# Optimization experiments

Measured on AMD Instinct MI355X. Metric: run time of the kernel, lower is better.

The kernel has to match this reference:

```python
import jax, jax.numpy as jnp
import numpy as np

DIM = 256
NUM_HEADS = 8
HEAD_DIM = DIM // NUM_HEADS
SCALE = HEAD_DIM ** (-0.5)


def setup_inputs() -> dict:
    key = jax.random.key(0)
    k1, k2, k3, k4 = jax.random.split(key, 4)
    x = jax.random.normal(k1, (4, 1, DIM, 12, 12, 12), dtype=jnp.float32)
    w_qkv = jax.random.normal(k2, (3 * DIM, DIM), dtype=jnp.float32) * 0.02
    w_proj = jax.random.normal(k3, (DIM, DIM), dtype=jnp.float32) * 0.02
    b_proj = jax.random.normal(k4, (DIM,), dtype=jnp.float32) * 0.02
    return {"x": x, "w_qkv": w_qkv, "w_proj": w_proj, "b_proj": b_proj}


def reference(x, w_qkv, w_proj, b_proj):
    # x: [P=4, B, C, H, W, D]; 1x1x1 Conv3d == channel matmul
    P, B, C, H, W, D = x.shape
    N = H * W * D
    xf = x.reshape(P, B, C, N)                       # [P,B,C,N]
    qkv = jnp.einsum('pbcn,oc->pbon', xf, w_qkv)     # [P,B,3C,N]
    q, k, v = jnp.split(qkv, 3, axis=2)              # each [P,B,C,N]
    # fold batch*heads
    def heads(t):
        return t.reshape(P, B * NUM_HEADS, HEAD_DIM, N)
    q, k, v = heads(q) * SCALE, heads(k), heads(v)
    attn = jnp.einsum('phcm,phcn->phmn', q, k)       # [P,BH,N,N]
    attn = jax.nn.softmax(attn, axis=-1)
    out = jnp.einsum('phmn,phcn->phcm', attn, v)     # [P,BH,hd,N]
    out = out.reshape(P, B, C, N)
    out = jnp.einsum('pbcn,oc->pbon', out, w_proj) + b_proj[None, None, :, None]
    return out.reshape(P, B, C, H, W, D)
```

## Files before the change

### kernel.cpp

```cpp
#include <hip/hip_runtime.h>

#define NP 4
#define NH 8
#define HD 32
#define CD 256
#define NN 1728
#define NT_TILES 27
#define SCALE_Q2 (0.17677669529663687f * 1.4426950408889634f)

typedef __bf16 bf16x8 __attribute__((ext_vector_type(8)));
typedef __bf16 bf16x4_t __attribute__((ext_vector_type(4)));
typedef short short4_t __attribute__((ext_vector_type(4)));
typedef float f32x4 __attribute__((ext_vector_type(4)));
typedef unsigned short ushort4_t __attribute__((ext_vector_type(4)));
typedef unsigned short ushort8_t __attribute__((ext_vector_type(8)));

__device__ __forceinline__ float bf2f(unsigned short u) {
  unsigned int v = ((unsigned int)u) << 16;
  return __builtin_bit_cast(float, v);
}
__device__ __forceinline__ unsigned short f2bf(float f) {
  unsigned int v = __builtin_bit_cast(unsigned int, f);
  unsigned int r = (v + 0x7FFFu + ((v >> 16) & 1u)) >> 16;
  return (unsigned short)r;
}

__global__ void k_prep(const float* __restrict__ x, unsigned short* __restrict__ xt,
                       const float* __restrict__ wqkv, const float* __restrict__ wproj,
                       unsigned short* __restrict__ wq_b, unsigned short* __restrict__ wp_b) {
  __shared__ __attribute__((aligned(16))) unsigned short tile[64 * 40];
  int bid = blockIdx.x;
  int t = threadIdx.x;
  if (bid >= 864) {
    int idx = ((bid - 864) * 256 + t) * 4;
    const float* src;
    unsigned short* dst;
    if (idx < 196608) { src = wqkv + idx; dst = wq_b + idx; }
    else { src = wproj + (idx - 196608); dst = wp_b + (idx - 196608); }
    float4 v = *(const float4*)src;
    ushort4_t o;
    o[0] = f2bf(v.x); o[1] = f2bf(v.y); o[2] = f2bf(v.z); o[3] = f2bf(v.w);
    *(ushort4_t*)dst = o;
    return;
  }
  int nb = (bid % 27) * 64, cb = ((bid / 27) & 7) * 32, p = bid / 216;
  {
    int c = t >> 3, ch = t & 7;
    const float* src = x + ((size_t)p * CD + cb + c) * NN + nb + ch * 8;
    float4 v0 = *(const float4*)src;
    float4 v1 = *(const float4*)(src + 4);
    int base = ch * 8;
    tile[(base + 0) * 40 + c] = f2bf(v0.x);
    tile[(base + 1) * 40 + c] = f2bf(v0.y);
    tile[(base + 2) * 40 + c] = f2bf(v0.z);
    tile[(base + 3) * 40 + c] = f2bf(v0.w);
    tile[(base + 4) * 40 + c] = f2bf(v1.x);
    tile[(base + 5) * 40 + c] = f2bf(v1.y);
    tile[(base + 6) * 40 + c] = f2bf(v1.z);
    tile[(base + 7) * 40 + c] = f2bf(v1.w);
  }
  __syncthreads();
  {
    int n = t >> 2, ch = t & 3;
    *(ushort8_t*)(xt + ((size_t)p * NN + nb + n) * CD + cb + ch * 8) =
        *(const ushort8_t*)&tile[n * 40 + ch * 8];
  }
}

__global__ void k_qkv(const unsigned short* __restrict__ xt,
                      const unsigned short* __restrict__ wqkv,
                      unsigned short* __restrict__ Qt, unsigned short* __restrict__ Kt,
                      unsigned short* __restrict__ Vv) {
  int p = blockIdx.z, ot = blockIdx.y, nt = blockIdx.x;
  int tid = threadIdx.x, w = tid >> 6, lane = tid & 63, l15 = lane & 15, g = lane >> 4;
  int nbase = nt * 64 + w * 16;
  f32x4 acc[4] = {};
  const unsigned short* arow = xt + ((size_t)p * NN + nbase + l15) * CD + g * 8;
  const unsigned short* wrow = wqkv + ((size_t)(ot * 64 + l15)) * CD + g * 8;
  for (int ks = 0; ks < 8; ks++) {
    bf16x8 a = *(const bf16x8*)(arow + ks * 32);
#pragma unroll
    for (int ob = 0; ob < 4; ob++) {
      bf16x8 b = *(const bf16x8*)(wrow + ob * 16 * CD + ks * 32);
      acc[ob] = __builtin_amdgcn_mfma_f32_16x16x32_bf16(a, b, acc[ob], 0, 0, 0);
    }
  }
#pragma unroll
  for (int ob = 0; ob < 4; ob++) {
    int o = ot * 64 + ob * 16 + l15;
    int wq = o >> 8, rem = o & 255, h = rem >> 5, cc = rem & 31;
    int ph = p * NH + h;
    int nrow = nbase + g * 4;
    if (wq == 0) {
      for (int r = 0; r < 4; r++)
        Qt[((size_t)ph * NN + nrow + r) * HD + cc] = f2bf(acc[ob][r] * SCALE_Q2);
    } else if (wq == 1) {
      for (int r = 0; r < 4; r++)
        Kt[((size_t)ph * NN + nrow + r) * HD + cc] = f2bf(acc[ob][r]);
    } else {
      ushort4_t vs;
      for (int r = 0; r < 4; r++) vs[r] = f2bf(acc[ob][r]);
      *(ushort4_t*)(Vv + ((size_t)ph * HD + cc) * NN + nrow) = vs;
    }
  }
}

__global__ __launch_bounds__(256) void k_attn(const unsigned short* __restrict__ Qt,
                                              const unsigned short* __restrict__ Kt,
                                              const unsigned short* __restrict__ Vv,
                                              unsigned short* __restrict__ op0,
                                              unsigned short* __restrict__ op1,
                                              float* __restrict__ Lp) {
  __shared__ __attribute__((aligned(16))) unsigned char lds[2 * (5120 + 4096)];
  int tid = threadIdx.x, w = tid >> 6, lane = tid & 63, l15 = lane & 15, g = lane >> 4;
  int mt = blockIdx.x, ph = blockIdx.y, z = blockIdx.z;
  int t0 = z * 14, tEnd = z ? NT_TILES : 14;
  const unsigned short* qptr = Qt + ((size_t)ph * NN + mt * 64 + w * 16 + l15) * HD + g * 8;
  bf16x8 qfrag = *(const bf16x8*)qptr;
  const unsigned short* ktb = Kt + (size_t)ph * NN * HD;
  const unsigned short* vb = Vv + (size_t)ph * HD * NN;
  f32x4 lsum = {0.f, 0.f, 0.f, 0.f};
  f32x4 oacc[2] = {};
  int snl = tid >> 2, sch = tid & 3;
  int svc = tid >> 3, svch = tid & 7;
  const int kst_off = snl * 80 + sch * 16;
  const int vst_off = (svc * 128 + svch * 16) ^ ((svc & 7) << 4);
  f32x4 zacc = {0.f, 0.f, 0.f, 0.f};
  {
    ushort8_t kr = *(const ushort8_t*)(ktb + ((size_t)(t0 * 64 + snl)) * HD + sch * 8);
    ushort8_t vr = *(const ushort8_t*)(vb + (size_t)svc * NN + t0 * 64 + svch * 8);
    *(ushort8_t*)(lds + kst_off) = kr;
    *(ushort8_t*)(lds + 5120 + vst_off) = vr;
  }
  __syncthreads();
  for (int nt = t0; nt < tEnd; nt++) {
    unsigned char* kbuf = lds + (nt & 1) * 9216;
    unsigned char* vbuf = kbuf + 5120;
    unsigned char* kbufN = lds + ((nt + 1) & 1) * 9216;
    unsigned char* vbufN = kbufN + 5120;
    ushort8_t kr, vr;
    bool pre = (nt + 1 < tEnd);
    if (pre) {
      kr = *(const ushort8_t*)(ktb + ((size_t)((nt + 1) * 64 + snl)) * HD + sch * 8);
      vr = *(const ushort8_t*)(vb + (size_t)svc * NN + (nt + 1) * 64 + svch * 8);
    }
    f32x4 s[4];
#pragma unroll
    for (int nf = 0; nf < 4; nf++) {
      bf16x8 kb = *(const bf16x8*)(kbuf + (nf * 16 + l15) * 80 + g * 16);
      s[nf] = __builtin_amdgcn_mfma_f32_16x16x32_bf16(kb, qfrag, zacc, 0, 0, 0);
    }
    short4_t pa[4];
#pragma unroll
    for (int nf = 0; nf < 4; nf++) {
      f32x4 e;
#pragma unroll
      for (int r = 0; r < 4; r++) e[r] = __builtin_amdgcn_exp2f(s[nf][r]);
      lsum += e;
      bf16x4_t t;
#pragma unroll
      for (int r = 0; r < 4; r++) t[r] = (__bf16)e[r];
      pa[nf] = __builtin_bit_cast(short4_t, t);
    }
#pragma unroll
    for (int nf = 0; nf < 4; nf++) {
#pragma unroll
      for (int cb = 0; cb < 2; cb++) {
        int c = cb * 16 + l15;
        ushort4_t vq = *(const ushort4_t*)(vbuf + ((c * 128 + nf * 32 + g * 8) ^ ((c & 7) << 4)));
        short4_t va = __builtin_bit_cast(short4_t, vq);
        oacc[cb] = __builtin_amdgcn_mfma_f32_16x16x16bf16_1k(va, pa[nf], oacc[cb], 0, 0, 0);
      }
    }
    if (pre) {
      *(ushort8_t*)(kbufN + kst_off) = kr;
      *(ushort8_t*)(vbufN + vst_off) = vr;
    }
    __syncthreads();
  }
  float total = lsum[0] + lsum[1] + lsum[2] + lsum[3];
  total += __shfl_xor(total, 16);
  total += __shfl_xor(total, 32);
  int m = mt * 64 + w * 16 + l15;
  unsigned short* op = z ? op1 : op0;
  if (g == 0) Lp[(size_t)z * 32 * NN + (size_t)ph * NN + m] = total;
#pragma unroll
  for (int cb = 0; cb < 2; cb++) {
    ushort4_t vs;
#pragma unroll
    for (int rr = 0; rr < 4; rr++) vs[rr] = f2bf(oacc[cb][rr]);
    *(ushort4_t*)(op + ((size_t)ph * NN + m) * 32 + cb * 16 + g * 4) = vs;
  }
}

__global__ void k_proj(const unsigned short* __restrict__ op0,
                       const unsigned short* __restrict__ op1,
                       const float* __restrict__ Lp,
                       const unsigned short* __restrict__ wproj,
                       const float* __restrict__ bproj,
                       float* __restrict__ out) {
  int p = blockIdx.z, ot = blockIdx.y, nt = blockIdx.x;
  int tid = threadIdx.x, w = tid >> 6, lane = tid & 63, l15 = lane & 15, g = lane >> 4;
  int nbase = nt * 64 + w * 16;
  int n = nbase + l15;
  f32x4 acc[4] = {};
  const unsigned short* wrow = wproj + ((size_t)(ot * 64 + l15)) * CD + g * 8;
  for (int ks = 0; ks < 8; ks++) {
    size_t r = (size_t)(p * NH + ks) * NN + n;
    float inv = 1.0f / (Lp[r] + Lp[(size_t)32 * NN + r]);
    ushort8_t a0 = *(const ushort8_t*)(op0 + r * 32 + g * 8);
    ushort8_t a1 = *(const ushort8_t*)(op1 + r * 32 + g * 8);
    bf16x8 a;
#pragma unroll
    for (int j = 0; j < 8; j++) a[j] = (__bf16)((bf2f(a0[j]) + bf2f(a1[j])) * inv);
#pragma unroll
    for (int ob = 0; ob < 4; ob++) {
      bf16x8 b = *(const bf16x8*)(wrow + ob * 16 * CD + ks * 32);
      acc[ob] = __builtin_amdgcn_mfma_f32_16x16x32_bf16(a, b, acc[ob], 0, 0, 0);
    }
  }
#pragma unroll
  for (int ob = 0; ob < 4; ob++) {
    int o = ot * 64 + ob * 16 + l15;
    float bias = bproj[o];
    int nrow = nbase + g * 4;
    float4 vs;
    vs.x = acc[ob][0] + bias;
    vs.y = acc[ob][1] + bias;
    vs.z = acc[ob][2] + bias;
    vs.w = acc[ob][3] + bias;
    *(float4*)(out + (size_t)p * CD * NN + (size_t)o * NN + nrow) = vs;
  }
}

extern "C" void kernel_launch(void* const* d_in, const int* in_sizes, int n_in,
                              void* d_out, int out_size, void* d_ws, size_t ws_size,
                              hipStream_t stream) {
  const float* x = (const float*)d_in[0];
  const float* wqkv = (const float*)d_in[1];
  const float* wproj = (const float*)d_in[2];
  const float* bproj = (const float*)d_in[3];
  float* out = (float*)d_out;
  unsigned short* ws = (unsigned short*)d_ws;
  const size_t SZ = (size_t)NP * NN * CD;
  unsigned short* xt = ws;
  unsigned short* Qt = ws + SZ;
  unsigned short* Kt = ws + 2 * SZ;
  unsigned short* Vv = ws + 3 * SZ;
  unsigned short* op1 = ws + 4 * SZ;
  unsigned short* wq_b = ws + 5 * SZ;
  unsigned short* wp_b = ws + 5 * SZ + 196608;
  float* Lp = (float*)(ws + 5 * SZ + 262144);
  unsigned short* op0 = xt;
  hipLaunchKernelGGL(k_prep, dim3(1120), dim3(256), 0, stream, x, xt, wqkv, wproj, wq_b, wp_b);
  hipLaunchKernelGGL(k_qkv, dim3(27, 12, NP), dim3(256), 0, stream, xt, wq_b, Qt, Kt, Vv);
  hipLaunchKernelGGL(k_attn, dim3(27, 32, 2), dim3(256), 0, stream, Qt, Kt, Vv, op0, op1, Lp);
  hipLaunchKernelGGL(k_proj, dim3(27, 4, NP), dim3(256), 0, stream, op0, op1, Lp, wp_b, bproj, out);
}
```

Baseline: 80.20 us.

## Store V in MFMA fragment order and read K/V straight from global

The QKV projection now writes V in a tiled layout that matches the MFMA operand fragment order. The attention kernel drops its LDS double buffer and its per-tile __syncthreads, and loads K and V fragments directly from global memory, relying on cache since all four waves read the same tiles. This removes the LDS staging and barriers, but adds latency-exposed global loads inside the loop with no explicit prefetch.

```diff
diff --git a/kernel.cpp b/kernel.cpp
--- a/kernel.cpp
+++ b/kernel.cpp
@@ -100,7 +100,7 @@
     } else {
       ushort4_t vs;
       for (int r = 0; r < 4; r++) vs[r] = f2bf(acc[ob][r]);
-      *(ushort4_t*)(Vv + ((size_t)ph * HD + cc) * NN + nrow) = vs;
+      *(ushort4_t*)(Vv + (size_t)ph * 55296 + nt * 2048 + w * 512 + cc * 16 + g * 4) = vs;
     }
   }
 }
@@ -111,43 +111,21 @@
                                               unsigned short* __restrict__ op0,
                                               unsigned short* __restrict__ op1,
                                               float* __restrict__ Lp) {
-  __shared__ __attribute__((aligned(16))) unsigned char lds[2 * (5120 + 4096)];
   int tid = threadIdx.x, w = tid >> 6, lane = tid & 63, l15 = lane & 15, g = lane >> 4;
   int mt = blockIdx.x, ph = blockIdx.y, z = blockIdx.z;
   int t0 = z * 14, tEnd = z ? NT_TILES : 14;
   const unsigned short* qptr = Qt + ((size_t)ph * NN + mt * 64 + w * 16 + l15) * HD + g * 8;
   bf16x8 qfrag = *(const bf16x8*)qptr;
   const unsigned short* ktb = Kt + (size_t)ph * NN * HD;
-  const unsigned short* vb = Vv + (size_t)ph * HD * NN;
+  const unsigned short* vb = Vv + (size_t)ph * 55296;
   f32x4 lsum = {0.f, 0.f, 0.f, 0.f};
   f32x4 oacc[2] = {};
-  int snl = tid >> 2, sch = tid & 3;
-  int svc = tid >> 3, svch = tid & 7;
-  const int kst_off = snl * 80 + sch * 16;
-  const int vst_off = (svc * 128 + svch * 16) ^ ((svc & 7) << 4);
   f32x4 zacc = {0.f, 0.f, 0.f, 0.f};
-  {
-    ushort8_t kr = *(const ushort8_t*)(ktb + ((size_t)(t0 * 64 + snl)) * HD + sch * 8);
-    ushort8_t vr = *(const ushort8_t*)(vb + (size_t)svc * NN + t0 * 64 + svch * 8);
-    *(ushort8_t*)(lds + kst_off) = kr;
-    *(ushort8_t*)(lds + 5120 + vst_off) = vr;
-  }
-  __syncthreads();
   for (int nt = t0; nt < tEnd; nt++) {
-    unsigned char* kbuf = lds + (nt & 1) * 9216;
-    unsigned char* vbuf = kbuf + 5120;
-    unsigned char* kbufN = lds + ((nt + 1) & 1) * 9216;
-    unsigned char* vbufN = kbufN + 5120;
-    ushort8_t kr, vr;
-    bool pre = (nt + 1 < tEnd);
-    if (pre) {
-      kr = *(const ushort8_t*)(ktb + ((size_t)((nt + 1) * 64 + snl)) * HD + sch * 8);
-      vr = *(const ushort8_t*)(vb + (size_t)svc * NN + (nt + 1) * 64 + svch * 8);
-    }
     f32x4 s[4];
 #pragma unroll
     for (int nf = 0; nf < 4; nf++) {
-      bf16x8 kb = *(const bf16x8*)(kbuf + (nf * 16 + l15) * 80 + g * 16);
+      bf16x8 kb = *(const bf16x8*)(ktb + ((size_t)(nt * 64 + nf * 16 + l15)) * HD + g * 8);
       s[nf] = __builtin_amdgcn_mfma_f32_16x16x32_bf16(kb, qfrag, zacc, 0, 0, 0);
     }
     short4_t pa[4];
@@ -162,21 +140,16 @@
       for (int r = 0; r < 4; r++) t[r] = (__bf16)e[r];
       pa[nf] = __builtin_bit_cast(short4_t, t);
     }
+    const unsigned short* vt = vb + nt * 2048;
 #pragma unroll
     for (int nf = 0; nf < 4; nf++) {
 #pragma unroll
       for (int cb = 0; cb < 2; cb++) {
-        int c = cb * 16 + l15;
-        ushort4_t vq = *(const ushort4_t*)(vbuf + ((c * 128 + nf * 32 + g * 8) ^ ((c & 7) << 4)));
+        ushort4_t vq = *(const ushort4_t*)(vt + nf * 512 + (cb * 16 + l15) * 16 + g * 4);
         short4_t va = __builtin_bit_cast(short4_t, vq);
         oacc[cb] = __builtin_amdgcn_mfma_f32_16x16x16bf16_1k(va, pa[nf], oacc[cb], 0, 0, 0);
       }
     }
-    if (pre) {
-      *(ushort8_t*)(kbufN + kst_off) = kr;
-      *(ushort8_t*)(vbufN + vst_off) = vr;
-    }
-    __syncthreads();
   }
   float total = lsum[0] + lsum[1] + lsum[2] + lsum[3];
   total += __shfl_xor(total, 16);
```

New measurement: 98.30 us. +22.6%, slower.
